# Optimization experiments

Hardware: AMD Instinct MI355X
Metric: run time of the kernel (lower is better)

Reference implementation:

```python
import jax, jax.numpy as jnp
import numpy as np
import math

IN_FEATURES = 512
RFF_FEATURES = 2048
OUT_FEATURES = 1000
N = 8192
RIDGE_PENALTY = 1.0
MEAN_FIELD_FACTOR = 25.0
RFF_SCALAR = math.sqrt(RFF_FEATURES / 2)  # 32.0


def _random_ortho(key, n, m):
    q, _ = jnp.linalg.qr(jax.random.normal(key, (n, m), dtype=jnp.float32))
    return q


def setup_inputs() -> dict:
    key = jax.random.key(0)
    k_d, k_w, k_norm, k_b, k_lw, k_lb, k_cov = jax.random.split(key, 7)
    D = jax.random.normal(k_d, (N, IN_FEATURES), dtype=jnp.float32)
    # RFF weight: concat of random orthonormal blocks (rff_features > in_features)
    ws = []
    dim_left = RFF_FEATURES
    kk = k_w
    while dim_left > IN_FEATURES:
        kk, sub = jax.random.split(kk)
        ws.append(_random_ortho(sub, IN_FEATURES, IN_FEATURES))
        dim_left -= IN_FEATURES
    kk, sub = jax.random.split(kk)
    ws.append(_random_ortho(sub, IN_FEATURES, dim_left))
    W = jnp.concatenate(ws, axis=1)  # [in, rff]
    feature_norm = jax.random.normal(k_norm, W.shape, dtype=jnp.float32) ** 2
    W = W * jnp.sqrt(feature_norm.sum(0))
    b = jax.random.uniform(k_b, (RFF_FEATURES,), dtype=jnp.float32) * (2.0 * math.pi)
    # logit head (nn.Linear): weight [out, rff], bias [out]
    bound = 1.0 / math.sqrt(RFF_FEATURES)
    logit_w = jax.random.uniform(k_lw, (OUT_FEATURES, RFF_FEATURES), dtype=jnp.float32,
                                 minval=-bound, maxval=bound)
    logit_b = jax.random.uniform(k_lb, (OUT_FEATURES,), dtype=jnp.float32,
                                 minval=-bound, maxval=bound)
    # positive-definite covariance buffer (stand-in for inverted precision)
    A = jax.random.normal(k_cov, (RFF_FEATURES, RFF_FEATURES), dtype=jnp.float32) * 0.01
    covariance = A @ A.T + jnp.eye(RFF_FEATURES, dtype=jnp.float32)
    return {"D": D, "W": W, "b": b, "logit_w": logit_w, "logit_b": logit_b,
            "covariance": covariance}


def reference(D, W, b, logit_w, logit_b, covariance):
    # RFF feature map: cos(D @ W + b) / rff_scalar  -> [N, rff]
    Phi = jnp.cos(D @ W + b) / RFF_SCALAR
    # linear head -> [N, out]
    pred = Phi @ logit_w.T + logit_b
    # diag(Phi @ cov @ Phi.T) * ridge computed row-wise in O(N*r^2)
    diag_cov = jnp.sum((Phi @ covariance) * Phi, axis=-1) * RIDGE_PENALTY  # [N]
    logits_scale = jnp.sqrt(1.0 + diag_cov * MEAN_FIELD_FACTOR)
    return pred / logits_scale[:, None]
```

## Files before the change

kernel.cpp:

```cpp
#include <hip/hip_runtime.h>
#include <math.h>

#define N_ROWS 8192
#define IN_F   512
#define RFF    2048
#define OUT_F  1000
#define OUT_PAD 1024
#define INV_RFF_SCALAR 0.03125f
#define MEAN_FIELD 25.0f

typedef __attribute__((ext_vector_type(8))) short short8;
typedef __attribute__((ext_vector_type(4))) float f32x4;

__device__ __forceinline__ unsigned short f32_to_bf16(float f) {
    unsigned u = __float_as_uint(f);
    unsigned r = 0x7FFFu + ((u >> 16) & 1u);
    return (unsigned short)((u + r) >> 16);
}
__device__ __forceinline__ float bf16_to_f32(unsigned short h) {
    return __uint_as_float(((unsigned)h) << 16);
}

__device__ __forceinline__ const uint4* gsrc(const unsigned short* X, int ldx,
                                             int r0, int k0, int q) {
    int rt = q >> 6, L = q & 63;
    int r = r0 + rt * 16 + (L & 15);
    int k = k0 + ((L >> 4) << 3);
    return (const uint4*)(X + (size_t)r * ldx + k);
}

__device__ __forceinline__ void stage_tile(const unsigned short* __restrict__ X, int ldx,
                                           int r0, int k0, unsigned short* lds,
                                           int w, int lane) {
    #pragma unroll
    for (int half = 0; half < 2; ++half) {
        int qb = half * 256 + w * 64;
        const uint4* g = gsrc(X, ldx, r0, k0, qb + lane);
        __builtin_amdgcn_global_load_lds(
            (const __attribute__((address_space(1))) void*)g,
            (__attribute__((address_space(3))) void*)(lds + qb * 8),
            16, 0, 0);
    }
}

__global__ __launch_bounds__(256) void conv_split_kernel(
    const float* __restrict__ X, unsigned short* __restrict__ H,
    unsigned short* __restrict__ L, int n4)
{
    int i = blockIdx.x * 256 + threadIdx.x;
    if (i >= n4) return;
    float4 v = ((const float4*)X)[i];
    ushort4 h, l;
    h.x = f32_to_bf16(v.x); l.x = f32_to_bf16(v.x - bf16_to_f32(h.x));
    h.y = f32_to_bf16(v.y); l.y = f32_to_bf16(v.y - bf16_to_f32(h.y));
    h.z = f32_to_bf16(v.z); l.z = f32_to_bf16(v.z - bf16_to_f32(h.z));
    h.w = f32_to_bf16(v.w); l.w = f32_to_bf16(v.w - bf16_to_f32(h.w));
    ((ushort4*)H)[i] = h;
    ((ushort4*)L)[i] = l;
}

__global__ __launch_bounds__(256) void conv_covu_kernel(
    const float* __restrict__ X, unsigned short* __restrict__ O)
{
    int i = blockIdx.x * 256 + threadIdx.x;
    int base = i * 4;
    int row = base >> 11;
    int col = base & 2047;
    int bn = row >> 7, bk = col >> 7;
    float w = (bk < bn) ? 1.0f : (bk == bn ? 0.5f : 0.0f);
    float4 v = ((const float4*)X)[i];
    ushort4 o;
    o.x = f32_to_bf16(v.x * w); o.y = f32_to_bf16(v.y * w);
    o.z = f32_to_bf16(v.z * w); o.w = f32_to_bf16(v.w * w);
    ((ushort4*)O)[i] = o;
}

__global__ __launch_bounds__(256) void conv_lw_kernel(
    const float* __restrict__ Lw, unsigned short* __restrict__ O)
{
    int i = blockIdx.x * 256 + threadIdx.x;
    int base = i * 4;
    int row = base >> 11;
    ushort4 o;
    if (row < OUT_F) {
        float4 v = ((const float4*)Lw)[i];
        o.x = f32_to_bf16(v.x); o.y = f32_to_bf16(v.y);
        o.z = f32_to_bf16(v.z); o.w = f32_to_bf16(v.w);
    } else {
        o.x = o.y = o.z = o.w = 0;
    }
    ((ushort4*)O)[i] = o;
}

__global__ __launch_bounds__(256) void conv_wt_kernel(
    const float* __restrict__ W, unsigned short* __restrict__ TH,
    unsigned short* __restrict__ TL)
{
    __shared__ float tile[64][65];
    const int tid = threadIdx.x;
    const int n0 = blockIdx.x * 64;
    const int k0 = blockIdx.y * 64;
    #pragma unroll
    for (int i = 0; i < 16; ++i) {
        int e = i * 256 + tid;
        int r = e >> 6, c = e & 63;
        tile[r][c] = W[(size_t)(k0 + r) * RFF + n0 + c];
    }
    __syncthreads();
    #pragma unroll
    for (int i = 0; i < 16; ++i) {
        int e = i * 256 + tid;
        int r = e >> 6, c = e & 63;
        float v = tile[c][r];
        unsigned short h = f32_to_bf16(v);
        unsigned short l = f32_to_bf16(v - bf16_to_f32(h));
        TH[(size_t)(n0 + r) * IN_F + k0 + c] = h;
        TL[(size_t)(n0 + r) * IN_F + k0 + c] = l;
    }
}

__global__ __launch_bounds__(256) void phi_mfma_kernel(
    const unsigned short* __restrict__ Dh, const unsigned short* __restrict__ Dl,
    const unsigned short* __restrict__ Wth, const unsigned short* __restrict__ Wtl,
    const float* __restrict__ bias, unsigned short* __restrict__ Phi)
{
    __shared__ unsigned short ldsAh[4096], ldsAl[4096], ldsBh[4096], ldsBl[4096];
    const int tid = threadIdx.x;
    const int w = tid >> 6, lane = tid & 63;
    const int wm = w >> 1, wn = w & 1;
    const int r0 = blockIdx.y * 128;
    const int c0 = blockIdx.x * 128;

    f32x4 acc[4][4];
    #pragma unroll
    for (int i = 0; i < 4; ++i)
        #pragma unroll
        for (int j = 0; j < 4; ++j)
            acc[i][j] = (f32x4)(0.0f);

    for (int k0 = 0; k0 < IN_F; k0 += 32) {
        __syncthreads();
        stage_tile(Dh,  IN_F, r0, k0, ldsAh, w, lane);
        stage_tile(Dl,  IN_F, r0, k0, ldsAl, w, lane);
        stage_tile(Wth, IN_F, c0, k0, ldsBh, w, lane);
        stage_tile(Wtl, IN_F, c0, k0, ldsBl, w, lane);
        __syncthreads();

        short8 fah[4], fal[4], fbh[4], fbl[4];
        #pragma unroll
        for (int t = 0; t < 4; ++t) {
            fah[t] = *(const short8*)(ldsAh + ((wm * 4 + t) * 64 + lane) * 8);
            fal[t] = *(const short8*)(ldsAl + ((wm * 4 + t) * 64 + lane) * 8);
            fbh[t] = *(const short8*)(ldsBh + ((wn * 4 + t) * 64 + lane) * 8);
            fbl[t] = *(const short8*)(ldsBl + ((wn * 4 + t) * 64 + lane) * 8);
        }
        #pragma unroll
        for (int mt = 0; mt < 4; ++mt)
            #pragma unroll
            for (int nt = 0; nt < 4; ++nt) {
                acc[mt][nt] = __builtin_amdgcn_mfma_f32_16x16x32_bf16(
                    fah[mt], fbh[nt], acc[mt][nt], 0, 0, 0);
                acc[mt][nt] = __builtin_amdgcn_mfma_f32_16x16x32_bf16(
                    fah[mt], fbl[nt], acc[mt][nt], 0, 0, 0);
                acc[mt][nt] = __builtin_amdgcn_mfma_f32_16x16x32_bf16(
                    fal[mt], fbh[nt], acc[mt][nt], 0, 0, 0);
            }
    }

    const int quad = lane >> 4, ln = lane & 15;
    #pragma unroll
    for (int mt = 0; mt < 4; ++mt)
        #pragma unroll
        for (int nt = 0; nt < 4; ++nt) {
            int col = c0 + wn * 64 + nt * 16 + ln;
            float bv = bias[col];
            #pragma unroll
            for (int reg = 0; reg < 4; ++reg) {
                int row = r0 + wm * 64 + mt * 16 + quad * 4 + reg;
                float z = acc[mt][nt][reg] + bv;
                float p = __cosf(z) * INV_RFF_SCALAR;
                Phi[(size_t)row * RFF + col] = f32_to_bf16(p);
            }
        }
}

__global__ __launch_bounds__(256) void diag_mfma_kernel(
    const unsigned short* __restrict__ Phi, const unsigned short* __restrict__ CovU,
    float* __restrict__ diag)
{
    __shared__ unsigned short ldsA[4096], ldsB[4096];
    const int tid = threadIdx.x;
    const int w = tid >> 6, lane = tid & 63;
    const int wm = w >> 1, wn = w & 1;
    const int J = (RFF / 128 - 1) - blockIdx.y;
    const int r0 = blockIdx.x * 128;
    const int c0 = J * 128;
    const int kmax = (J + 1) * 128;

    f32x4 acc[4][4];
    #pragma unroll
    for (int i = 0; i < 4; ++i)
        #pragma unroll
        for (int j = 0; j < 4; ++j)
            acc[i][j] = (f32x4)(0.0f);

    for (int k0 = 0; k0 < kmax; k0 += 32) {
        __syncthreads();
        stage_tile(Phi,  RFF, r0, k0, ldsA, w, lane);
        stage_tile(CovU, RFF, c0, k0, ldsB, w, lane);
        __syncthreads();

        short8 fa[4], fb[4];
        #pragma unroll
        for (int t = 0; t < 4; ++t) {
            fa[t] = *(const short8*)(ldsA + ((wm * 4 + t) * 64 + lane) * 8);
            fb[t] = *(const short8*)(ldsB + ((wn * 4 + t) * 64 + lane) * 8);
        }
        #pragma unroll
        for (int mt = 0; mt < 4; ++mt)
            #pragma unroll
            for (int nt = 0; nt < 4; ++nt)
                acc[mt][nt] = __builtin_amdgcn_mfma_f32_16x16x32_bf16(
                    fa[mt], fb[nt], acc[mt][nt], 0, 0, 0);
    }

    const int quad = lane >> 4, ln = lane & 15;
    #pragma unroll
    for (int mt = 0; mt < 4; ++mt) {
        float psum[4] = {0.f, 0.f, 0.f, 0.f};
        #pragma unroll
        for (int nt = 0; nt < 4; ++nt) {
            int col = c0 + wn * 64 + nt * 16 + ln;
            #pragma unroll
            for (int reg = 0; reg < 4; ++reg) {
                int row = r0 + wm * 64 + mt * 16 + quad * 4 + reg;
                float pv = bf16_to_f32(Phi[(size_t)row * RFF + col]);
                psum[reg] = fmaf(acc[mt][nt][reg], pv, psum[reg]);
            }
        }
        #pragma unroll
        for (int off = 1; off < 16; off <<= 1)
            #pragma unroll
            for (int reg = 0; reg < 4; ++reg)
                psum[reg] += __shfl_xor(psum[reg], off, 16);
        if (ln == 0) {
            #pragma unroll
            for (int reg = 0; reg < 4; ++reg) {
                int row = r0 + wm * 64 + mt * 16 + quad * 4 + reg;
                atomicAdd(&diag[row], 2.0f * psum[reg]);
            }
        }
    }
}

__global__ __launch_bounds__(256) void pred_mfma_kernel(
    const unsigned short* __restrict__ Phi, const unsigned short* __restrict__ Lw,
    const float* __restrict__ Lb, const float* __restrict__ diag,
    float* __restrict__ out)
{
    __shared__ unsigned short ldsA[4096], ldsB[4096];
    const int tid = threadIdx.x;
    const int w = tid >> 6, lane = tid & 63;
    const int wm = w >> 1, wn = w & 1;
    const int r0 = blockIdx.y * 128;
    const int c0 = blockIdx.x * 128;

    f32x4 acc[4][4];
    #pragma unroll
    for (int i = 0; i < 4; ++i)
        #pragma unroll
        for (int j = 0; j < 4; ++j)
            acc[i][j] = (f32x4)(0.0f);

    for (int k0 = 0; k0 < RFF; k0 += 32) {
        __syncthreads();
        stage_tile(Phi, RFF, r0, k0, ldsA, w, lane);
        stage_tile(Lw,  RFF, c0, k0, ldsB, w, lane);
        __syncthreads();

        short8 fa[4], fb[4];
        #pragma unroll
        for (int t = 0; t < 4; ++t) {
            fa[t] = *(const short8*)(ldsA + ((wm * 4 + t) * 64 + lane) * 8);
            fb[t] = *(const short8*)(ldsB + ((wn * 4 + t) * 64 + lane) * 8);
        }
        #pragma unroll
        for (int mt = 0; mt < 4; ++mt)
            #pragma unroll
            for (int nt = 0; nt < 4; ++nt)
                acc[mt][nt] = __builtin_amdgcn_mfma_f32_16x16x32_bf16(
                    fa[mt], fb[nt], acc[mt][nt], 0, 0, 0);
    }

    const int quad = lane >> 4, ln = lane & 15;
    #pragma unroll
    for (int mt = 0; mt < 4; ++mt) {
        float s[4];
        #pragma unroll
        for (int reg = 0; reg < 4; ++reg) {
            int row = r0 + wm * 64 + mt * 16 + quad * 4 + reg;
            s[reg] = 1.0f / sqrtf(1.0f + MEAN_FIELD * diag[row]);
        }
        #pragma unroll
        for (int nt = 0; nt < 4; ++nt) {
            int col = c0 + wn * 64 + nt * 16 + ln;
            if (col < OUT_F) {
                float bv = Lb[col];
                #pragma unroll
                for (int reg = 0; reg < 4; ++reg) {
                    int row = r0 + wm * 64 + mt * 16 + quad * 4 + reg;
                    out[(size_t)row * OUT_F + col] = (acc[mt][nt][reg] + bv) * s[reg];
                }
            }
        }
    }
}

extern "C" void kernel_launch(void* const* d_in, const int* in_sizes, int n_in,
                              void* d_out, int out_size, void* d_ws, size_t ws_size,
                              hipStream_t stream) {
    const float* D    = (const float*)d_in[0];
    const float* W    = (const float*)d_in[1];
    const float* bias = (const float*)d_in[2];
    const float* Lw   = (const float*)d_in[3];
    const float* Lb   = (const float*)d_in[4];
    const float* cov  = (const float*)d_in[5];
    float* out = (float*)d_out;

    char* p = (char*)d_ws;
    unsigned short* Phi16 = (unsigned short*)p;                 p += (size_t)N_ROWS * RFF * 2;
    unsigned short* Dh    = (unsigned short*)p;                 p += (size_t)N_ROWS * IN_F * 2;
    unsigned short* Dl    = (unsigned short*)p;                 p += (size_t)N_ROWS * IN_F * 2;
    unsigned short* Wth   = (unsigned short*)p;                 p += (size_t)RFF * IN_F * 2;
    unsigned short* Wtl   = (unsigned short*)p;                 p += (size_t)RFF * IN_F * 2;
    unsigned short* Lw16  = (unsigned short*)p;                 p += (size_t)OUT_PAD * RFF * 2;
    unsigned short* CovU  = (unsigned short*)p;                 p += (size_t)RFF * RFF * 2;
    float* diag           = (float*)p;

    hipMemsetAsync(diag, 0, N_ROWS * sizeof(float), stream);

    dim3 blk(256);
    conv_split_kernel<<<dim3((N_ROWS * IN_F / 4 + 255) / 256), blk, 0, stream>>>(D, Dh, Dl, N_ROWS * IN_F / 4);
    conv_wt_kernel<<<dim3(RFF / 64, IN_F / 64), blk, 0, stream>>>(W, Wth, Wtl);
    conv_lw_kernel<<<dim3(OUT_PAD * RFF / 4 / 256), blk, 0, stream>>>(Lw, Lw16);
    conv_covu_kernel<<<dim3(RFF * RFF / 4 / 256), blk, 0, stream>>>(cov, CovU);

    phi_mfma_kernel<<<dim3(RFF / 128, N_ROWS / 128), blk, 0, stream>>>(Dh, Dl, Wth, Wtl, bias, Phi16);
    diag_mfma_kernel<<<dim3(N_ROWS / 128, RFF / 128), blk, 0, stream>>>(Phi16, CovU, diag);
    pred_mfma_kernel<<<dim3(OUT_PAD / 128, N_ROWS / 128), blk, 0, stream>>>(Phi16, Lw16, Lb, diag, out);
}
```

Before: 322.3 us.

## Use FP8 for covariance quadratic form and co-schedule diag with pred GEMM

Computes the Phi·Cov·Phi diagonal with FP8 MFMA on scaled Phi and a triangular covariance, whose diagonal is zeroed and restored in FP32 in the epilogue. The diag and prediction GEMMs are merged into one interleaved launch so they run concurrently, and the per-row scale moves into a separate pass over the output. This roughly halves operand bytes and raises MFMA throughput for the larger GEMM, but adds an FP8 conversion pass and an extra read-modify-write of the output, and lowers precision of the uncertainty term.

```diff
diff --git a/kernel.cpp b/kernel.cpp
--- a/kernel.cpp
+++ b/kernel.cpp
@@ -1,4 +1,5 @@
 #include <hip/hip_runtime.h>
+#include <hip/hip_fp8.h>
 #include <math.h>
 
 #define N_ROWS 8192
@@ -20,6 +21,10 @@
 __device__ __forceinline__ float bf16_to_f32(unsigned short h) {
     return __uint_as_float(((unsigned)h) << 16);
 }
+__device__ __forceinline__ unsigned char f32_to_fp8(float x) {
+    __hip_fp8_e4m3 q(x);
+    return (unsigned char)q.__x;
+}
 
 __device__ __forceinline__ const uint4* gsrc(const unsigned short* X, int ldx,
                                              int r0, int k0, int q) {
@@ -39,6 +44,24 @@
         __builtin_amdgcn_global_load_lds(
             (const __attribute__((address_space(1))) void*)g,
             (__attribute__((address_space(3))) void*)(lds + qb * 8),
+            16, 0, 0);
+    }
+}
+
+__device__ __forceinline__ void stage_tile8(const unsigned char* __restrict__ X, int ldb,
+                                            int r0, int k0b, unsigned char* lds,
+                                            int w, int lane) {
+    #pragma unroll
+    for (int half = 0; half < 2; ++half) {
+        int qb = half * 256 + w * 64;
+        int q = qb + lane;
+        int rt = q >> 6, L = q & 63;
+        int row = r0 + rt * 16 + (L & 15);
+        int kb = k0b + ((L >> 4) << 4);
+        const void* g = X + (size_t)row * ldb + kb;
+        __builtin_amdgcn_global_load_lds(
+            (const __attribute__((address_space(1))) void*)g,
+            (__attribute__((address_space(3))) void*)(lds + qb * 16),
             16, 0, 0);
     }
 }
@@ -59,20 +82,44 @@
     ((ushort4*)L)[i] = l;
 }
 
-__global__ __launch_bounds__(256) void conv_covu_kernel(
-    const float* __restrict__ X, unsigned short* __restrict__ O)
+__global__ __launch_bounds__(256) void conv_covu8_kernel(
+    const float* __restrict__ X, unsigned char* __restrict__ O)
 {
     int i = blockIdx.x * 256 + threadIdx.x;
     int base = i * 4;
     int row = base >> 11;
     int col = base & 2047;
     int bn = row >> 7, bk = col >> 7;
-    float w = (bk < bn) ? 1.0f : (bk == bn ? 0.5f : 0.0f);
+    float w = (bk < bn) ? 16.0f : (bk == bn ? 8.0f : 0.0f);
     float4 v = ((const float4*)X)[i];
-    ushort4 o;
-    o.x = f32_to_bf16(v.x * w); o.y = f32_to_bf16(v.y * w);
-    o.z = f32_to_bf16(v.z * w); o.w = f32_to_bf16(v.w * w);
-    ((ushort4*)O)[i] = o;
+    float w0 = (col + 0 == row) ? 0.0f : w;
+    float w1 = (col + 1 == row) ? 0.0f : w;
+    float w2 = (col + 2 == row) ? 0.0f : w;
+    float w3 = (col + 3 == row) ? 0.0f : w;
+    uchar4 o;
+    o.x = f32_to_fp8(v.x * w0); o.y = f32_to_fp8(v.y * w1);
+    o.z = f32_to_fp8(v.z * w2); o.w = f32_to_fp8(v.w * w3);
+    ((uchar4*)O)[i] = o;
+}
+
+__global__ __launch_bounds__(256) void conv_covd_kernel(
+    const float* __restrict__ X, float* __restrict__ Cd)
+{
+    int i = blockIdx.x * 256 + threadIdx.x;
+    if (i < RFF) Cd[i] = X[(size_t)i * RFF + i];
+}
+
+__global__ __launch_bounds__(256) void conv_phi8_kernel(
+    const unsigned short* __restrict__ Phi16, unsigned char* __restrict__ Phi8)
+{
+    int i = blockIdx.x * 256 + threadIdx.x;
+    ushort4 v = ((const ushort4*)Phi16)[i];
+    uchar4 o;
+    o.x = f32_to_fp8(bf16_to_f32(v.x) * 32.0f);
+    o.y = f32_to_fp8(bf16_to_f32(v.y) * 32.0f);
+    o.z = f32_to_fp8(bf16_to_f32(v.z) * 32.0f);
+    o.w = f32_to_fp8(bf16_to_f32(v.w) * 32.0f);
+    ((uchar4*)Phi8)[i] = o;
 }
 
 __global__ __launch_bounds__(256) void conv_lw_kernel(
@@ -184,18 +231,18 @@
         }
 }
 
-__global__ __launch_bounds__(256) void diag_mfma_kernel(
-    const unsigned short* __restrict__ Phi, const unsigned short* __restrict__ CovU,
-    float* __restrict__ diag)
-{
-    __shared__ unsigned short ldsA[4096], ldsB[4096];
+__global__ __launch_bounds__(256) void fused_dp_kernel(
+    const unsigned short* __restrict__ Phi16, const unsigned char* __restrict__ Phi8,
+    const unsigned char* __restrict__ CovU8, const float* __restrict__ Cd,
+    const unsigned short* __restrict__ Lw, const float* __restrict__ Lb,
+    float* __restrict__ diag, float* __restrict__ out)
+{
+    __shared__ __align__(16) unsigned char smem[16384];
     const int tid = threadIdx.x;
     const int w = tid >> 6, lane = tid & 63;
     const int wm = w >> 1, wn = w & 1;
-    const int J = (RFF / 128 - 1) - blockIdx.y;
-    const int r0 = blockIdx.x * 128;
-    const int c0 = J * 128;
-    const int kmax = (J + 1) * 128;
+    const int quad = lane >> 4, ln = lane & 15;
+    const int b = blockIdx.x;
 
     f32x4 acc[4][4];
     #pragma unroll
@@ -204,115 +251,125 @@
         for (int j = 0; j < 4; ++j)
             acc[i][j] = (f32x4)(0.0f);
 
-    for (int k0 = 0; k0 < kmax; k0 += 32) {
-        __syncthreads();
-        stage_tile(Phi,  RFF, r0, k0, ldsA, w, lane);
-        stage_tile(CovU, RFF, c0, k0, ldsB, w, lane);
-        __syncthreads();
-
-        short8 fa[4], fb[4];
-        #pragma unroll
-        for (int t = 0; t < 4; ++t) {
-            fa[t] = *(const short8*)(ldsA + ((wm * 4 + t) * 64 + lane) * 8);
-            fb[t] = *(const short8*)(ldsB + ((wn * 4 + t) * 64 + lane) * 8);
+    if (b % 3 != 2) {
+        const int d = (b / 3) * 2 + (b % 3);
+        const int J = 15 - (d >> 6);
+        const int r0 = (d & 63) * 128;
+        const int c0 = J * 128;
+        const int kmaxb = (J + 1) * 128;
+        unsigned char* ldsA8 = smem;
+        unsigned char* ldsB8 = smem + 8192;
+
+        for (int k0b = 0; k0b < kmaxb; k0b += 64) {
+            __syncthreads();
+            stage_tile8(Phi8,  RFF, r0, k0b, ldsA8, w, lane);
+            stage_tile8(CovU8, RFF, c0, k0b, ldsB8, w, lane);
+            __syncthreads();
+
+            #pragma unroll
+            for (int s = 0; s < 2; ++s) {
+                const int ccol = s * 2 + (quad >> 1);
+                const int off8 = (quad & 1) << 3;
+                long fa[4], fb[4];
+                #pragma unroll
+                for (int t = 0; t < 4; ++t) {
+                    fa[t] = *(const long*)(ldsA8 + (((wm * 4 + t) * 64 + ccol * 16 + ln) << 4) + off8);
+                    fb[t] = *(const long*)(ldsB8 + (((wn * 4 + t) * 64 + ccol * 16 + ln) << 4) + off8);
+                }
+                #pragma unroll
+                for (int mt = 0; mt < 4; ++mt)
+                    #pragma unroll
+                    for (int nt = 0; nt < 4; ++nt)
+                        acc[mt][nt] = __builtin_amdgcn_mfma_f32_16x16x32_fp8_fp8(
+                            fa[mt], fb[nt], acc[mt][nt], 0, 0, 0);
+            }
         }
-        #pragma unroll
-        for (int mt = 0; mt < 4; ++mt)
-            #pragma unroll
-            for (int nt = 0; nt < 4; ++nt)
-                acc[mt][nt] = __builtin_amdgcn_mfma_f32_16x16x32_bf16(
-                    fa[mt], fb[nt], acc[mt][nt], 0, 0, 0);
-    }
-
-    const int quad = lane >> 4, ln = lane & 15;
-    #pragma unroll
-    for (int mt = 0; mt < 4; ++mt) {
-        float psum[4] = {0.f, 0.f, 0.f, 0.f};
-        #pragma unroll
-        for (int nt = 0; nt < 4; ++nt) {
-            int col = c0 + wn * 64 + nt * 16 + ln;
-            #pragma unroll
-            for (int reg = 0; reg < 4; ++reg) {
-                int row = r0 + wm * 64 + mt * 16 + quad * 4 + reg;
-                float pv = bf16_to_f32(Phi[(size_t)row * RFF + col]);
-                psum[reg] = fmaf(acc[mt][nt][reg], pv, psum[reg]);
-            }
-        }
-        #pragma unroll
-        for (int off = 1; off < 16; off <<= 1)
-            #pragma unroll
-            for (int reg = 0; reg < 4; ++reg)
-                psum[reg] += __shfl_xor(psum[reg], off, 16);
-        if (ln == 0) {
-            #pragma unroll
-            for (int reg = 0; reg < 4; ++reg) {
-                int row = r0 + wm * 64 + mt * 16 + quad * 4 + reg;
-                atomicAdd(&diag[row], 2.0f * psum[reg]);
-            }
-        }
-    }
-}
-
-__global__ __launch_bounds__(256) void pred_mfma_kernel(
-    const unsigned short* __restrict__ Phi, const unsigned short* __restrict__ Lw,
-    const float* __restrict__ Lb, const float* __restrict__ diag,
-    float* __restrict__ out)
-{
-    __shared__ unsigned short ldsA[4096], ldsB[4096];
-    const int tid = threadIdx.x;
-    const int w = tid >> 6, lane = tid & 63;
-    const int wm = w >> 1, wn = w & 1;
-    const int r0 = blockIdx.y * 128;
-    const int c0 = blockIdx.x * 128;
-
-    f32x4 acc[4][4];
-    #pragma unroll
-    for (int i = 0; i < 4; ++i)
-        #pragma unroll
-        for (int j = 0; j < 4; ++j)
-            acc[i][j] = (f32x4)(0.0f);
-
-    for (int k0 = 0; k0 < RFF; k0 += 32) {
-        __syncthreads();
-        stage_tile(Phi, RFF, r0, k0, ldsA, w, lane);
-        stage_tile(Lw,  RFF, c0, k0, ldsB, w, lane);
-        __syncthreads();
-
-        short8 fa[4], fb[4];
-        #pragma unroll
-        for (int t = 0; t < 4; ++t) {
-            fa[t] = *(const short8*)(ldsA + ((wm * 4 + t) * 64 + lane) * 8);
-            fb[t] = *(const short8*)(ldsB + ((wn * 4 + t) * 64 + lane) * 8);
-        }
-        #pragma unroll
-        for (int mt = 0; mt < 4; ++mt)
-            #pragma unroll
-            for (int nt = 0; nt < 4; ++nt)
-                acc[mt][nt] = __builtin_amdgcn_mfma_f32_16x16x32_bf16(
-                    fa[mt], fb[nt], acc[mt][nt], 0, 0, 0);
-    }
-
-    const int quad = lane >> 4, ln = lane & 15;
-    #pragma unroll
-    for (int mt = 0; mt < 4; ++mt) {
-        float s[4];
-        #pragma unroll
-        for (int reg = 0; reg < 4; ++reg) {
-            int row = r0 + wm * 64 + mt * 16 + quad * 4 + reg;
-            s[reg] = 1.0f / sqrtf(1.0f + MEAN_FIELD * diag[row]);
-        }
-        #pragma unroll
-        for (int nt = 0; nt < 4; ++nt) {
-            int col = c0 + wn * 64 + nt * 16 + ln;
-            if (col < OUT_F) {
-                float bv = Lb[col];
+
+        float cd[4];
+        #pragma unroll
+        for (int nt = 0; nt < 4; ++nt)
+            cd[nt] = 256.0f * Cd[c0 + wn * 64 + nt * 16 + ln];
+        #pragma unroll
+        for (int mt = 0; mt < 4; ++mt) {
+            float psum[4] = {0.f, 0.f, 0.f, 0.f};
+            #pragma unroll
+            for (int nt = 0; nt < 4; ++nt) {
+                int col = c0 + wn * 64 + nt * 16 + ln;
                 #pragma unroll
                 for (int reg = 0; reg < 4; ++reg) {
                     int row = r0 + wm * 64 + mt * 16 + quad * 4 + reg;
-                    out[(size_t)row * OUT_F + col] = (acc[mt][nt][reg] + bv) * s[reg];
+                    float pv = bf16_to_f32(Phi16[(size_t)row * RFF + col]);
+                    psum[reg] = fmaf(fmaf(cd[nt], pv, acc[mt][nt][reg]), pv, psum[reg]);
                 }
             }
+            #pragma unroll
+            for (int off = 1; off < 16; off <<= 1)
+                #pragma unroll
+                for (int reg = 0; reg < 4; ++reg)
+                    psum[reg] += __shfl_xor(psum[reg], off, 16);
+            if (ln == 0) {
+                #pragma unroll
+                for (int reg = 0; reg < 4; ++reg) {
+                    int row = r0 + wm * 64 + mt * 16 + quad * 4 + reg;
+                    atomicAdd(&diag[row], psum[reg] * (1.0f / 256.0f));
+                }
+            }
         }
+    } else {
+        const int p = b / 3;
+        const int r0 = (p >> 3) * 128;
+        const int c0 = (p & 7) * 128;
+        unsigned short* ldsA = (unsigned short*)smem;
+        unsigned short* ldsB = (unsigned short*)(smem + 8192);
+
+        for (int k0 = 0; k0 < RFF; k0 += 32) {
+            __syncthreads();
+            stage_tile(Phi16, RFF, r0, k0, ldsA, w, lane);
+            stage_tile(Lw,    RFF, c0, k0, ldsB, w, lane);
+            __syncthreads();
+
+            short8 fa[4], fb[4];
+            #pragma unroll
+            for (int t = 0; t < 4; ++t) {
+                fa[t] = *(const short8*)(ldsA + ((wm * 4 + t) * 64 + lane) * 8);
+                fb[t] = *(const short8*)(ldsB + ((wn * 4 + t) * 64 + lane) * 8);
+            }
+            #pragma unroll
+            for (int mt = 0; mt < 4; ++mt)
+                #pragma unroll
+                for (int nt = 0; nt < 4; ++nt)
+                    acc[mt][nt] = __builtin_amdgcn_mfma_f32_16x16x32_bf16(
+                        fa[mt], fb[nt], acc[mt][nt], 0, 0, 0);
+        }
+
+        #pragma unroll
+        for (int mt = 0; mt < 4; ++mt)
+            #pragma unroll
+            for (int nt = 0; nt < 4; ++nt) {
+                int col = c0 + wn * 64 + nt * 16 + ln;
+                if (col < OUT_F) {
+                    float bv = Lb[col];
+                    #pragma unroll
+                    for (int reg = 0; reg < 4; ++reg) {
+                        int row = r0 + wm * 64 + mt * 16 + quad * 4 + reg;
+                        out[(size_t)row * OUT_F + col] = acc[mt][nt][reg] + bv;
+                    }
+                }
+            }
+    }
+}
+
+__global__ __launch_bounds__(256) void scale_kernel(
+    float* __restrict__ out, const float* __restrict__ diag)
+{
+    const int row = blockIdx.x;
+    const int t = threadIdx.x;
+    float s = 1.0f / sqrtf(1.0f + MEAN_FIELD * diag[row]);
+    if (t < 250) {
+        float4* p = (float4*)(out + (size_t)row * OUT_F);
+        float4 v = p[t];
+        v.x *= s; v.y *= s; v.z *= s; v.w *= s;
+        p[t] = v;
     }
 }
 
@@ -328,13 +385,16 @@
     float* out = (float*)d_out;
 
     char* p = (char*)d_ws;
-    unsigned short* Phi16 = (unsigned short*)p;                 p += (size_t)N_ROWS * RFF * 2;
-    unsigned short* Dh    = (unsigned short*)p;                 p += (size_t)N_ROWS * IN_F * 2;
-    unsigned short* Dl    = (unsigned short*)p;                 p += (size_t)N_ROWS * IN_F * 2;
-    unsigned short* Wth   = (unsigned short*)p;                 p += (size_t)RFF * IN_F * 2;
-    unsigned short* Wtl   = (unsigned short*)p;                 p += (size_t)RFF * IN_F * 2;
-    unsigned short* Lw16  = (unsigned short*)p;                 p += (size_t)OUT_PAD * RFF * 2;
-    unsigned short* CovU  = (unsigned short*)p;                 p += (size_t)RFF * RFF * 2;
+    unsigned short* Phi16 = (unsigned short*)p;  p += (size_t)N_ROWS * RFF * 2;
+    unsigned char*  Phi8  = (unsigned char*)p;
+    unsigned short* Dh    = (unsigned short*)p;  p += (size_t)N_ROWS * IN_F * 2;
+    unsigned short* Dl    = (unsigned short*)p;  p += (size_t)N_ROWS * IN_F * 2;
+    unsigned short* Wth   = (unsigned short*)p;  p += (size_t)RFF * IN_F * 2;
+    unsigned short* Wtl   = (unsigned short*)p;  p += (size_t)RFF * IN_F * 2;
+    unsigned short* Lw16  = (unsigned short*)p;  p += (size_t)OUT_PAD * RFF * 2;
+    unsigned char*  CovU8 = (unsigned char*)p;
+    float*          Cd    = (float*)(p + (size_t)RFF * RFF);
+    p += (size_t)RFF * RFF * 2;
     float* diag           = (float*)p;
 
     hipMemsetAsync(diag, 0, N_ROWS * sizeof(float), stream);
@@ -343,9 +403,12 @@
     conv_split_kernel<<<dim3((N_ROWS * IN_F / 4 + 255) / 256), blk, 0, stream>>>(D, Dh, Dl, N_ROWS * IN_F / 4);
     conv_wt_kernel<<<dim3(RFF / 64, IN_F / 64), blk, 0, stream>>>(W, Wth, Wtl);
     conv_lw_kernel<<<dim3(OUT_PAD * RFF / 4 / 256), blk, 0, stream>>>(Lw, Lw16);
-    conv_covu_kernel<<<dim3(RFF * RFF / 4 / 256), blk, 0, stream>>>(cov, CovU);
+    conv_covu8_kernel<<<dim3(RFF * RFF / 4 / 256), blk, 0, stream>>>(cov, CovU8);
+    conv_covd_kernel<<<dim3(RFF / 256), blk, 0, stream>>>(cov, Cd);
 
     phi_mfma_kernel<<<dim3(RFF / 128, N_ROWS / 128), blk, 0, stream>>>(Dh, Dl, Wth, Wtl, bias, Phi16);
-    diag_mfma_kernel<<<dim3(N_ROWS / 128, RFF / 128), blk, 0, stream>>>(Phi16, CovU, diag);
-    pred_mfma_kernel<<<dim3(OUT_PAD / 128, N_ROWS / 128), blk, 0, stream>>>(Phi16, Lw16, Lb, diag, out);
-}
+    conv_phi8_kernel<<<dim3(N_ROWS * RFF / 4 / 256), blk, 0, stream>>>(Phi16, Phi8);
+
+    fused_dp_kernel<<<dim3(1536), blk, 0, stream>>>(Phi16, Phi8, CovU8, Cd, Lw16, Lb, diag, out);
+    scale_kernel<<<dim3(N_ROWS), blk, 0, stream>>>(out, diag);
+}
```

Measured after the change: 365.3 us. 13.3% more time.
